# Kernel tuning notes

Hardware: AMD Instinct MI355X
Metric: run time of the kernel (lower is better)

Reference implementation:

```python
import jax, jax.numpy as jnp
import numpy as np


def setup_inputs() -> dict:
    key = jax.random.key(0)
    k1, k2, k3, k4 = jax.random.split(key, 4)
    B, C, H, W = 4, 64, 128, 256
    Cout, kH, kW = 64, 3, 3
    x = jax.random.normal(k1, (B, C, H, W), dtype=jnp.float32)
    # offset layout: channel 2*(i*kW+j) = dy, 2*(i*kW+j)+1 = dx (deformable_groups=1)
    offset = jax.random.normal(k2, (B, 2 * kH * kW, H, W), dtype=jnp.float32)
    weight = jax.random.normal(k3, (Cout, C, kH, kW), dtype=jnp.float32) * 0.05
    bias = jax.random.normal(k4, (Cout,), dtype=jnp.float32) * 0.05
    return {"x": x, "offset": offset, "weight": weight, "bias": bias}


STRIDE, PAD, DIL = 1, 1, 1


def _deform_conv(x, offset, weight, bias):
    B, C, H, W = x.shape
    Cout, Cin, kH, kW = weight.shape
    K = kH * kW
    Ho = (H + 2 * PAD - DIL * (kH - 1) - 1) // STRIDE + 1
    Wo = (W + 2 * PAD - DIL * (kW - 1) - 1) // STRIDE + 1

    hs = (jnp.arange(Ho) * STRIDE - PAD).astype(jnp.float32)  # [Ho]
    ws = (jnp.arange(Wo) * STRIDE - PAD).astype(jnp.float32)  # [Wo]
    ki, kj = jnp.meshgrid(jnp.arange(kH), jnp.arange(kW), indexing="ij")
    ki = (ki.reshape(K) * DIL).astype(jnp.float32)  # [K]
    kj = (kj.reshape(K) * DIL).astype(jnp.float32)

    off = offset.reshape(B, K, 2, Ho, Wo)
    dy, dx = off[:, :, 0], off[:, :, 1]  # [B,K,Ho,Wo]
    py = hs[None, None, :, None] + ki[None, :, None, None] + dy  # [B,K,Ho,Wo]
    px = ws[None, None, None, :] + kj[None, :, None, None] + dx

    y0 = jnp.floor(py)
    x0 = jnp.floor(px)
    ly = py - y0
    lx = px - x0
    y0i = y0.astype(jnp.int32)
    x0i = x0.astype(jnp.int32)

    def gather(xb, yi, xi):
        # xb: [C,H,W]; yi, xi: [K,Ho,Wo]; zero for out-of-bounds corners
        valid = (yi >= 0) & (yi < H) & (xi >= 0) & (xi < W)
        yc = jnp.clip(yi, 0, H - 1)
        xc = jnp.clip(xi, 0, W - 1)
        idx = (yc * W + xc).reshape(-1)
        g = jnp.take(xb.reshape(C, H * W), idx, axis=1).reshape(C, K, Ho, Wo)
        return g * valid[None].astype(xb.dtype)

    gather_b = jax.vmap(gather)
    corners = [
        (y0i, x0i, (1.0 - ly) * (1.0 - lx)),
        (y0i, x0i + 1, (1.0 - ly) * lx),
        (y0i + 1, x0i, ly * (1.0 - lx)),
        (y0i + 1, x0i + 1, ly * lx),
    ]
    vals = jnp.zeros((B, C, K, Ho, Wo), dtype=x.dtype)
    for yi, xi, w in corners:
        vals = vals + gather_b(x, yi, xi) * w[:, None]  # broadcast over C

    out = jnp.einsum("bckhw,ock->bohw", vals, weight.reshape(Cout, Cin, K))
    return out + bias[None, :, None, None]


def reference(x, offset, weight, bias):
    return _deform_conv(x, offset, weight, bias)
```

## Files before the change

### kernel.cpp

```cpp
#include <hip/hip_runtime.h>

typedef float floatx4 __attribute__((ext_vector_type(4)));
typedef _Float16 half2v __attribute__((ext_vector_type(2)));
typedef _Float16 half8 __attribute__((ext_vector_type(8)));

#define Hh 128
#define Ww 256
#define Cc 64
#define COUT 64
#define Bb 4
#define HW (Hh*Ww)
#define VP 74

__launch_bounds__(512, 4)
__global__ void prep(const float* __restrict__ x, const float* __restrict__ wsrc,
                     _Float16* __restrict__ xn, unsigned short* __restrict__ wdst) {
    const int bid = blockIdx.x;
    const int tid = threadIdx.x;
    if (bid >= 512) {
        const int i = (bid - 512) * 72 + tid;
        if (tid < 72) {
            const int kt = i % 9, c = (i / 9) % Cc, o = i / (9 * Cc);
            const int mbh = o >> 5, mi = (o >> 4) & 1, r = o & 15;
            const int g = c >> 5, ks = (c >> 3) & 3, s = c & 7;
            const int ln = ks * 16 + r, j = g * 2 + mi;
            _Float16 hv = (_Float16)wsrc[i];
            wdst[(((kt * 2 + mbh) * 4 + j) * 64 + ln) * 8 + s] = *(unsigned short*)&hv;
        }
        return;
    }
    const int cg = bid >> 6;
    const int T  = bid & 63;
    const int b  = T >> 4;
    const int ht = T & 15;
    __shared__ float Tf[64][260];
    const float* src = x + ((size_t)(b * Cc + cg * 8) * Hh + ht * 8) * Ww;
#pragma unroll
    for (int s = 0; s < 8; ++s) {
        const int u   = s * 512 + tid;
        const int row = u >> 6;
        const int wq  = u & 63;
        const float4 v = *(const float4*)(src + (size_t)(row >> 3) * HW + (row & 7) * Ww + wq * 4);
        *(float4*)&Tf[row][wq * 4] = v;
    }
    __syncthreads();
#pragma unroll
    for (int j2 = 0; j2 < 4; ++j2) {
        const int idx = j2 * 512 + tid;
        const int hh = idx >> 8, w = idx & 255;
        unsigned o4[4];
#pragma unroll
        for (int cp = 0; cp < 4; ++cp) {
            half2v hv;
            hv.x = (_Float16)Tf[(2 * cp) * 8 + hh][w];
            hv.y = (_Float16)Tf[(2 * cp + 1) * 8 + hh][w];
            o4[cp] = *(unsigned*)&hv;
        }
        uint4 u4; u4.x = o4[0]; u4.y = o4[1]; u4.z = o4[2]; u4.w = o4[3];
        *(uint4*)(xn + ((size_t)(b * Hh + ht * 8 + hh) * Ww + w) * 64 + cg * 8) = u4;
    }
}

__device__ __forceinline__ void lds_barrier() {
    asm volatile("s_waitcnt lgkmcnt(0)\n\ts_barrier" ::: "memory");
}

struct Tap {
    half2v W00, W01, W10, W11;
    int a00, a01, a10, a11;
};

template<int I>
__device__ __forceinline__ unsigned (&sel3(unsigned (&a)[16], unsigned (&b)[16],
                                           unsigned (&c)[16]))[16] {
    if constexpr (I == 0) return a; else if constexpr (I == 1) return b; else return c;
}
template<int I>
__device__ __forceinline__ Tap& sel3t(Tap& a, Tap& b, Tap& c) {
    if constexpr (I == 0) return a; else if constexpr (I == 1) return b; else return c;
}

__device__ __forceinline__ void tap_setup(int kt, int h, int w, float dy, float dx,
                                          int cg, Tap& t) {
    const int ki = kt / 3, kj = kt % 3;
    const float py = (float)(h - 1 + ki) + dy;
    const float px = (float)(w - 1 + kj) + dx;
    const float y0f = floorf(py), x0f = floorf(px);
    const int y0 = (int)y0f, x0 = (int)x0f;
    const float ly = py - y0f, lx = px - x0f;
    const int y1 = y0 + 1, x1 = x0 + 1;
    const bool vy0 = ((unsigned)y0 < Hh), vy1 = ((unsigned)y1 < Hh);
    const bool vx0 = ((unsigned)x0 < Ww), vx1 = ((unsigned)x1 < Ww);
    const float w00 = (vy0 && vx0) ? (1.f - ly) * (1.f - lx) : 0.f;
    const float w01 = (vy0 && vx1) ? (1.f - ly) * lx : 0.f;
    const float w10 = (vy1 && vx0) ? ly * (1.f - lx) : 0.f;
    const float w11 = (vy1 && vx1) ? ly * lx : 0.f;
    _Float16 h00 = (_Float16)w00, h01 = (_Float16)w01;
    _Float16 h10 = (_Float16)w10, h11 = (_Float16)w11;
    t.W00.x = h00; t.W00.y = h00;  t.W01.x = h01; t.W01.y = h01;
    t.W10.x = h10; t.W10.y = h10;  t.W11.x = h11; t.W11.y = h11;
    const int y0c = min(max(y0, 0), Hh - 1), y1c = min(max(y1, 0), Hh - 1);
    const int x0c = min(max(x0, 0), Ww - 1), x1c = min(max(x1, 0), Ww - 1);
    t.a00 = (y0c * Ww + x0c) * 8 + cg;
    t.a01 = (y0c * Ww + x1c) * 8 + cg;
    t.a10 = (y1c * Ww + x0c) * 8 + cg;
    t.a11 = (y1c * Ww + x1c) * 8 + cg;
}

__device__ __forceinline__ void tap_load(const uint4* __restrict__ xb4, const Tap& t,
                                         unsigned (&pf)[16]) {
    *(uint4*)&pf[0]  = xb4[t.a00];
    *(uint4*)&pf[4]  = xb4[t.a01];
    *(uint4*)&pf[8]  = xb4[t.a10];
    *(uint4*)&pf[12] = xb4[t.a11];
}

__device__ __forceinline__ void wf_load(const unsigned short* __restrict__ wt,
                                        half8 (&WF)[4]) {
    WF[0] = *(const half8*)(wt);
    WF[1] = *(const half8*)(wt + 512);
    WF[2] = *(const half8*)(wt + 1024);
    WF[3] = *(const half8*)(wt + 1536);
}

__device__ __forceinline__ void tap_store(const Tap& t, const unsigned (&pf)[16],
                                          unsigned short* __restrict__ vrow) {
    unsigned o[4];
#pragma unroll
    for (int s = 0; s < 4; ++s) {
        half2v v = (*(const half2v*)&pf[s])      * t.W00
                 + (*(const half2v*)&pf[4 + s])  * t.W01
                 + (*(const half2v*)&pf[8 + s])  * t.W10
                 + (*(const half2v*)&pf[12 + s]) * t.W11;
        o[s] = *(unsigned*)&v;
    }
    uint4 u; u.x = o[0]; u.y = o[1]; u.z = o[2]; u.w = o[3];
    *(uint4*)vrow = u;
}

__device__ __forceinline__ void mfma_tap(const half8 (&WF)[4],
                                         const unsigned short* __restrict__ Vbuf,
                                         int nt, int ln, floatx4 (&acc)[2]) {
#pragma unroll
    for (int g = 0; g < 2; ++g) {
        const int pp = nt * 16 + (ln & 15);
        half8 bfrag = *(const half8*)&Vbuf[pp * VP + g * 32 + (ln >> 4) * 8];
        acc[0] = __builtin_amdgcn_mfma_f32_16x16x32_f16(WF[2 * g],     bfrag, acc[0], 0, 0, 0);
        acc[1] = __builtin_amdgcn_mfma_f32_16x16x32_f16(WF[2 * g + 1], bfrag, acc[1], 0, 0, 0);
    }
}

template<int KT>
__device__ __forceinline__ void pipe_iter(
    const uint4* __restrict__ xb4, const float* __restrict__ offb,
    const unsigned short* __restrict__ wfb,
    const unsigned short* __restrict__ V0, const unsigned short* __restrict__ V1,
    unsigned short* __restrict__ vrow0, unsigned short* __restrict__ vrow1,
    int h, int w, int cg, int nt, int ln,
    Tap& tpA, Tap& tpB, Tap& tpC,
    unsigned (&pfA)[16], unsigned (&pfB)[16], unsigned (&pfC)[16],
    half8 (&WF0)[4], half8 (&WF1)[4],
    float& dy0, float& dx0, float& dy1, float& dx1,
    floatx4 (&acc)[2])
{
    constexpr int S = KT & 1;
    wf_load(wfb + KT * 4096, S ? WF1 : WF0);
    if constexpr (KT + 2 <= 8) {
        constexpr int GI = (KT + 2) % 3;
        Tap& tg = sel3t<GI>(tpA, tpB, tpC);
        tap_setup(KT + 2, h, w, S ? dy1 : dy0, S ? dx1 : dx0, cg, tg);
        tap_load(xb4, tg, sel3<GI>(pfA, pfB, pfC));
    }
    if constexpr (KT + 4 <= 8) {
        (S ? dy1 : dy0) = offb[(2 * (KT + 4)) * HW];
        (S ? dx1 : dx0) = offb[(2 * (KT + 4) + 1) * HW];
    }
    constexpr int Tm = 1 - S;
    mfma_tap(Tm ? WF1 : WF0, Tm ? V1 : V0, nt, ln, acc);
    constexpr int SI = KT % 3;
    tap_store(sel3t<SI>(tpA, tpB, tpC), sel3<SI>(pfA, pfB, pfC),
              S ? vrow1 : vrow0);
    lds_barrier();
}

__launch_bounds__(256, 4)
__global__ void dcn_mfma(const _Float16* __restrict__ xn,
                         const float* __restrict__ offset,
                         const unsigned short* __restrict__ wb,
                         const float* __restrict__ bias,
                         float* __restrict__ out) {
    __shared__ unsigned short V[2][32 * VP];

    const int tid = threadIdx.x;
    const int p   = tid >> 3;
    const int cg  = tid & 7;
    const int wv  = tid >> 6;
    const int ln  = tid & 63;

    const int b  = blockIdx.z;
    const int h  = blockIdx.y;
    const int w0 = blockIdx.x * 32;
    const int w  = w0 + p;

    const uint4* xb4  = (const uint4*)(xn + (size_t)b * HW * 64);
    const float* offb = offset + b * 18 * HW + h * Ww + w;
    unsigned short* vrow0 = &V[0][p * VP + cg * 8];
    unsigned short* vrow1 = &V[1][p * VP + cg * 8];

    const int nt = wv & 1;
    const int mb = (wv >> 1) * 2;
    const unsigned short* wfb = wb + (wv >> 1) * 2048 + ln * 8;

    floatx4 acc[2];
    acc[0] = (floatx4)0.f; acc[1] = (floatx4)0.f;

    unsigned pfA[16], pfB[16], pfC[16];
    half8 WF0[4], WF1[4];
    Tap tpA, tpB, tpC;

    float dy0 = offb[0],        dx0 = offb[HW];
    float dy1 = offb[2 * HW],   dx1 = offb[3 * HW];
    wf_load(wfb, WF0);
    tap_setup(0, h, w, dy0, dx0, cg, tpA);
    tap_load(xb4, tpA, pfA);
    tap_setup(1, h, w, dy1, dx1, cg, tpB);
    tap_load(xb4, tpB, pfB);
    dy0 = offb[4 * HW]; dx0 = offb[5 * HW];
    dy1 = offb[6 * HW]; dx1 = offb[7 * HW];
    tap_setup(2, h, w, dy0, dx0, cg, tpC);
    tap_load(xb4, tpC, pfC);
    dy0 = offb[8 * HW]; dx0 = offb[9 * HW];
    tap_store(tpA, pfA, vrow0);
    lds_barrier();

#define PI(K) pipe_iter<K>(xb4, offb, wfb, V[0], V[1], vrow0, vrow1, h, w, cg, nt, ln, \
                           tpA, tpB, tpC, pfA, pfB, pfC, WF0, WF1,                     \
                           dy0, dx0, dy1, dx1, acc)
    PI(1); PI(2); PI(3); PI(4); PI(5); PI(6); PI(7); PI(8);
#undef PI

    mfma_tap(WF0, V[0], nt, ln, acc);

    float* outp = out + b * COUT * HW + h * Ww;
    const int col = w0 + nt * 16 + (ln & 15);
#pragma unroll
    for (int mi = 0; mi < 2; ++mi)
#pragma unroll
        for (int r = 0; r < 4; ++r) {
            const int o = (mb + mi) * 16 + (ln >> 4) * 4 + r;
            outp[o * HW + col] = acc[mi][r] + bias[o];
        }
}

extern "C" void kernel_launch(void* const* d_in, const int* in_sizes, int n_in,
                              void* d_out, int out_size, void* d_ws, size_t ws_size,
                              hipStream_t stream) {
    const float* x      = (const float*)d_in[0];
    const float* offset = (const float*)d_in[1];
    const float* weight = (const float*)d_in[2];
    const float* bias   = (const float*)d_in[3];
    float* out = (float*)d_out;

    _Float16* xn = (_Float16*)d_ws;
    unsigned short* wb = (unsigned short*)((char*)d_ws + (size_t)Bb * HW * Cc * 2);

    prep<<<dim3(1024), 512, 0, stream>>>(x, weight, xn, wb);
    dcn_mfma<<<dim3(Ww / 32, Hh, Bb), 256, 0, stream>>>(xn, offset, wb, bias, out);
}
```

Before: 143.7 us.

## Stage weights into LDS via global_load_lds and shorten tap prefetch depth

Weight fragments for each tap are now copied into a double-buffered LDS area with direct global-to-LDS loads, then read from LDS, instead of each wave loading them from global memory into registers. The tap gather pipeline drops from three in-flight tap buffers to two. Explicit vmcnt waits replace the compiler's own ordering. The goal is to cut register pressure and redundant global weight traffic. The cost is more LDS use and shallower gather latency hiding, and the hand-counted vmcnt values must match the loads actually in flight.

```diff
diff --git a/kernel.cpp b/kernel.cpp
--- a/kernel.cpp
+++ b/kernel.cpp
@@ -64,21 +64,14 @@
 __device__ __forceinline__ void lds_barrier() {
     asm volatile("s_waitcnt lgkmcnt(0)\n\ts_barrier" ::: "memory");
 }
+__device__ __forceinline__ void sched_fence() {
+    asm volatile("" ::: "memory");
+}
 
 struct Tap {
     half2v W00, W01, W10, W11;
     int a00, a01, a10, a11;
 };
-
-template<int I>
-__device__ __forceinline__ unsigned (&sel3(unsigned (&a)[16], unsigned (&b)[16],
-                                           unsigned (&c)[16]))[16] {
-    if constexpr (I == 0) return a; else if constexpr (I == 1) return b; else return c;
-}
-template<int I>
-__device__ __forceinline__ Tap& sel3t(Tap& a, Tap& b, Tap& c) {
-    if constexpr (I == 0) return a; else if constexpr (I == 1) return b; else return c;
-}
 
 __device__ __forceinline__ void tap_setup(int kt, int h, int w, float dy, float dx,
                                           int cg, Tap& t) {
@@ -115,12 +108,25 @@
     *(uint4*)&pf[12] = xb4[t.a11];
 }
 
-__device__ __forceinline__ void wf_load(const unsigned short* __restrict__ wt,
+__device__ __forceinline__ void gll16(const unsigned short* g, unsigned short* l) {
+    __builtin_amdgcn_global_load_lds(
+        (const __attribute__((address_space(1))) unsigned int*)g,
+        (__attribute__((address_space(3))) unsigned int*)l, 16, 0, 0);
+}
+__device__ __forceinline__ void stage_w(const unsigned short* __restrict__ wb, int kt,
+                                        unsigned short* ldsbuf, int wv, int ln) {
+    sched_fence();
+    gll16(wb + kt * 4096 + wv * 1024 + ln * 8,       ldsbuf + wv * 1024);
+    gll16(wb + kt * 4096 + wv * 1024 + 512 + ln * 8, ldsbuf + wv * 1024 + 512);
+    sched_fence();
+}
+
+__device__ __forceinline__ void wf_read(const unsigned short* __restrict__ wl,
                                         half8 (&WF)[4]) {
-    WF[0] = *(const half8*)(wt);
-    WF[1] = *(const half8*)(wt + 512);
-    WF[2] = *(const half8*)(wt + 1024);
-    WF[3] = *(const half8*)(wt + 1536);
+    WF[0] = *(const half8*)(wl);
+    WF[1] = *(const half8*)(wl + 512);
+    WF[2] = *(const half8*)(wl + 1024);
+    WF[3] = *(const half8*)(wl + 1536);
 }
 
 __device__ __forceinline__ void tap_store(const Tap& t, const unsigned (&pf)[16],
@@ -150,37 +156,35 @@
     }
 }
 
-template<int KT>
+template<int J>
 __device__ __forceinline__ void pipe_iter(
     const uint4* __restrict__ xb4, const float* __restrict__ offb,
-    const unsigned short* __restrict__ wfb,
+    const unsigned short* __restrict__ wb,
+    unsigned short (&WL)[2][4096],
     const unsigned short* __restrict__ V0, const unsigned short* __restrict__ V1,
     unsigned short* __restrict__ vrow0, unsigned short* __restrict__ vrow1,
-    int h, int w, int cg, int nt, int ln,
-    Tap& tpA, Tap& tpB, Tap& tpC,
-    unsigned (&pfA)[16], unsigned (&pfB)[16], unsigned (&pfC)[16],
+    int h, int w, int cg, int nt, int ln, int wv,
+    Tap& tp0, Tap& tp1, unsigned (&pf0)[16], unsigned (&pf1)[16],
     half8 (&WF0)[4], half8 (&WF1)[4],
     float& dy0, float& dx0, float& dy1, float& dx1,
     floatx4 (&acc)[2])
 {
-    constexpr int S = KT & 1;
-    wf_load(wfb + KT * 4096, S ? WF1 : WF0);
-    if constexpr (KT + 2 <= 8) {
-        constexpr int GI = (KT + 2) % 3;
-        Tap& tg = sel3t<GI>(tpA, tpB, tpC);
-        tap_setup(KT + 2, h, w, S ? dy1 : dy0, S ? dx1 : dx0, cg, tg);
-        tap_load(xb4, tg, sel3<GI>(pfA, pfB, pfC));
-    }
-    if constexpr (KT + 4 <= 8) {
-        (S ? dy1 : dy0) = offb[(2 * (KT + 4)) * HW];
-        (S ? dx1 : dx0) = offb[(2 * (KT + 4) + 1) * HW];
-    }
-    constexpr int Tm = 1 - S;
-    mfma_tap(Tm ? WF1 : WF0, Tm ? V1 : V0, nt, ln, acc);
-    constexpr int SI = KT % 3;
-    tap_store(sel3t<SI>(tpA, tpB, tpC), sel3<SI>(pfA, pfB, pfC),
-              S ? vrow1 : vrow0);
+    constexpr int S = J & 1, P = 1 - S;
+    if constexpr (J + 1 <= 8) {
+        tap_setup(J + 1, h, w, P ? dy1 : dy0, P ? dx1 : dx0, cg, P ? tp1 : tp0);
+        tap_load(xb4, P ? tp1 : tp0, P ? pf1 : pf0);
+    }
+    if constexpr (J + 3 <= 8) {
+        (P ? dy1 : dy0) = offb[(2 * (J + 3)) * HW];
+        (P ? dx1 : dx0) = offb[(2 * (J + 3) + 1) * HW];
+    }
+    constexpr int NVM = (J + 1 <= 8 ? 4 : 0) + (J + 3 <= 8 ? 2 : 0);
+    asm volatile("s_waitcnt vmcnt(%0)" :: "n"(NVM) : "memory");
     lds_barrier();
+    wf_read(&WL[S][(wv >> 1) * 2048 + ln * 8], S ? WF1 : WF0);
+    if constexpr (J + 1 <= 8) stage_w(wb, J + 1, WL[P], wv, ln);
+    mfma_tap(P ? WF1 : WF0, P ? V1 : V0, nt, ln, acc);
+    tap_store(S ? tp1 : tp0, S ? pf1 : pf0, S ? vrow1 : vrow0);
 }
 
 __launch_bounds__(256, 4)
@@ -190,6 +194,7 @@
                          const float* __restrict__ bias,
                          float* __restrict__ out) {
     __shared__ unsigned short V[2][32 * VP];
+    __shared__ unsigned short WL[2][4096];
 
     const int tid = threadIdx.x;
     const int p   = tid >> 3;
@@ -209,36 +214,35 @@
 
     const int nt = wv & 1;
     const int mb = (wv >> 1) * 2;
-    const unsigned short* wfb = wb + (wv >> 1) * 2048 + ln * 8;
 
     floatx4 acc[2];
     acc[0] = (floatx4)0.f; acc[1] = (floatx4)0.f;
 
-    unsigned pfA[16], pfB[16], pfC[16];
+    unsigned pf0[16], pf1[16];
     half8 WF0[4], WF1[4];
-    Tap tpA, tpB, tpC;
+    Tap tp0, tp1;
 
     float dy0 = offb[0],        dx0 = offb[HW];
     float dy1 = offb[2 * HW],   dx1 = offb[3 * HW];
-    wf_load(wfb, WF0);
-    tap_setup(0, h, w, dy0, dx0, cg, tpA);
-    tap_load(xb4, tpA, pfA);
-    tap_setup(1, h, w, dy1, dx1, cg, tpB);
-    tap_load(xb4, tpB, pfB);
+    stage_w(wb, 0, WL[0], wv, ln);
+    tap_setup(0, h, w, dy0, dx0, cg, tp0);
+    tap_load(xb4, tp0, pf0);
     dy0 = offb[4 * HW]; dx0 = offb[5 * HW];
+    tap_setup(1, h, w, dy1, dx1, cg, tp1);
+    tap_load(xb4, tp1, pf1);
     dy1 = offb[6 * HW]; dx1 = offb[7 * HW];
-    tap_setup(2, h, w, dy0, dx0, cg, tpC);
-    tap_load(xb4, tpC, pfC);
-    dy0 = offb[8 * HW]; dx0 = offb[9 * HW];
-    tap_store(tpA, pfA, vrow0);
+    asm volatile("s_waitcnt vmcnt(12)" ::: "memory");
     lds_barrier();
-
-#define PI(K) pipe_iter<K>(xb4, offb, wfb, V[0], V[1], vrow0, vrow1, h, w, cg, nt, ln, \
-                           tpA, tpB, tpC, pfA, pfB, pfC, WF0, WF1,                     \
-                           dy0, dx0, dy1, dx1, acc)
+    wf_read(&WL[0][(wv >> 1) * 2048 + ln * 8], WF0);
+    stage_w(wb, 1, WL[1], wv, ln);
+    tap_store(tp0, pf0, vrow0);
+
+#define PI(K) pipe_iter<K>(xb4, offb, wb, WL, V[0], V[1], vrow0, vrow1, h, w, cg, nt, ln, wv, \
+                           tp0, tp1, pf0, pf1, WF0, WF1, dy0, dx0, dy1, dx1, acc)
     PI(1); PI(2); PI(3); PI(4); PI(5); PI(6); PI(7); PI(8);
 #undef PI
 
+    lds_barrier();
     mfma_tap(WF0, V[0], nt, ln, acc);
 
     float* outp = out + b * COUT * HW + h * Ww;
```

After: 150.3 us. +4.6%, slower.

## Use four LDS tap buffers so barriers are needed only every other tap

Applied to the files above, without the earlier changes.

Expands the shared-memory staging buffer from two slots to four. The MFMA consumer now lags two taps behind the producer, so the block-wide barrier runs only after odd taps, halving barrier count. Weight fragment loads shift accordingly, with an extra register set holding the last tap's weights. This costs more LDS per block, which could reduce occupancy, and more registers.

```diff
diff --git a/kernel.cpp b/kernel.cpp
--- a/kernel.cpp
+++ b/kernel.cpp
@@ -154,17 +154,17 @@
 __device__ __forceinline__ void pipe_iter(
     const uint4* __restrict__ xb4, const float* __restrict__ offb,
     const unsigned short* __restrict__ wfb,
-    const unsigned short* __restrict__ V0, const unsigned short* __restrict__ V1,
-    unsigned short* __restrict__ vrow0, unsigned short* __restrict__ vrow1,
+    unsigned short (&V)[4][32 * VP], int vrow_off,
     int h, int w, int cg, int nt, int ln,
     Tap& tpA, Tap& tpB, Tap& tpC,
     unsigned (&pfA)[16], unsigned (&pfB)[16], unsigned (&pfC)[16],
-    half8 (&WF0)[4], half8 (&WF1)[4],
+    half8 (&WF0)[4], half8 (&WF1)[4], half8 (&WFe)[4],
     float& dy0, float& dx0, float& dy1, float& dx1,
     floatx4 (&acc)[2])
 {
     constexpr int S = KT & 1;
-    wf_load(wfb + KT * 4096, S ? WF1 : WF0);
+    wf_load(wfb + (KT - 1) * 4096, ((KT - 1) & 1) ? WF1 : WF0);
+    if constexpr (KT == 8) wf_load(wfb + 8 * 4096, WFe);
     if constexpr (KT + 2 <= 8) {
         constexpr int GI = (KT + 2) % 3;
         Tap& tg = sel3t<GI>(tpA, tpB, tpC);
@@ -175,12 +175,13 @@
         (S ? dy1 : dy0) = offb[(2 * (KT + 4)) * HW];
         (S ? dx1 : dx0) = offb[(2 * (KT + 4) + 1) * HW];
     }
-    constexpr int Tm = 1 - S;
-    mfma_tap(Tm ? WF1 : WF0, Tm ? V1 : V0, nt, ln, acc);
+    if constexpr (KT >= 2) {
+        mfma_tap(((KT - 2) & 1) ? WF1 : WF0, V[(KT - 2) & 3], nt, ln, acc);
+    }
     constexpr int SI = KT % 3;
     tap_store(sel3t<SI>(tpA, tpB, tpC), sel3<SI>(pfA, pfB, pfC),
-              S ? vrow1 : vrow0);
-    lds_barrier();
+              V[KT & 3] + vrow_off);
+    if constexpr (KT & 1) lds_barrier();
 }
 
 __launch_bounds__(256, 4)
@@ -189,7 +190,7 @@
                          const unsigned short* __restrict__ wb,
                          const float* __restrict__ bias,
                          float* __restrict__ out) {
-    __shared__ unsigned short V[2][32 * VP];
+    __shared__ unsigned short V[4][32 * VP];
 
     const int tid = threadIdx.x;
     const int p   = tid >> 3;
@@ -204,8 +205,7 @@
 
     const uint4* xb4  = (const uint4*)(xn + (size_t)b * HW * 64);
     const float* offb = offset + b * 18 * HW + h * Ww + w;
-    unsigned short* vrow0 = &V[0][p * VP + cg * 8];
-    unsigned short* vrow1 = &V[1][p * VP + cg * 8];
+    const int vrow_off = p * VP + cg * 8;
 
     const int nt = wv & 1;
     const int mb = (wv >> 1) * 2;
@@ -215,12 +215,11 @@
     acc[0] = (floatx4)0.f; acc[1] = (floatx4)0.f;
 
     unsigned pfA[16], pfB[16], pfC[16];
-    half8 WF0[4], WF1[4];
+    half8 WF0[4], WF1[4], WFe[4];
     Tap tpA, tpB, tpC;
 
     float dy0 = offb[0],        dx0 = offb[HW];
     float dy1 = offb[2 * HW],   dx1 = offb[3 * HW];
-    wf_load(wfb, WF0);
     tap_setup(0, h, w, dy0, dx0, cg, tpA);
     tap_load(xb4, tpA, pfA);
     tap_setup(1, h, w, dy1, dx1, cg, tpB);
@@ -230,16 +229,17 @@
     tap_setup(2, h, w, dy0, dx0, cg, tpC);
     tap_load(xb4, tpC, pfC);
     dy0 = offb[8 * HW]; dx0 = offb[9 * HW];
-    tap_store(tpA, pfA, vrow0);
-    lds_barrier();
-
-#define PI(K) pipe_iter<K>(xb4, offb, wfb, V[0], V[1], vrow0, vrow1, h, w, cg, nt, ln, \
-                           tpA, tpB, tpC, pfA, pfB, pfC, WF0, WF1,                     \
+    tap_store(tpA, pfA, V[0] + vrow_off);
+
+#define PI(K) pipe_iter<K>(xb4, offb, wfb, V, vrow_off, h, w, cg, nt, ln, \
+                           tpA, tpB, tpC, pfA, pfB, pfC, WF0, WF1, WFe,   \
                            dy0, dx0, dy1, dx1, acc)
     PI(1); PI(2); PI(3); PI(4); PI(5); PI(6); PI(7); PI(8);
 #undef PI
 
-    mfma_tap(WF0, V[0], nt, ln, acc);
+    lds_barrier();
+    mfma_tap(WF1, V[3], nt, ln, acc);
+    mfma_tap(WFe, V[0], nt, ln, acc);
 
     float* outp = out + b * COUT * HW + h * Ww;
     const int col = w0 + nt * 16 + (ln & 15);
```

Measured after the change: 145.1 us. No clear change (+1.0%).
